# Performance work log

Hardware: AMD Instinct MI355X
Metric: run time of the kernel (lower is better)

## Reference

```python
import jax, jax.numpy as jnp
import numpy as np


def setup_inputs() -> dict:
    key = jax.random.key(0)
    k1, k2, k3 = jax.random.split(key, 3)
    B, C, H, W = 16, 256, 32, 32
    D, K = 256, 8192
    x = jax.random.normal(k1, (B, C, H, W), dtype=jnp.float32)
    conv_w = jax.random.normal(k2, (D, C), dtype=jnp.float32) * (1.0 / np.sqrt(C))
    conv_b = jnp.zeros((D,), dtype=jnp.float32)
    codebook = jax.random.normal(k3, (D, K), dtype=jnp.float32)
    return {"x": x, "conv_w": conv_w, "conv_b": conv_b, "codebook": codebook}


def reference(x, conv_w, conv_b, codebook):
    # 1x1 conv projection: (B,C,H,W) -> (B,D,H,W)
    xp = jnp.einsum('bchw,dc->bdhw', x, conv_w) + conv_b[None, :, None, None]
    B, D, H, W = xp.shape
    K = codebook.shape[1]
    # flatten to (N, D), N = B*H*W
    xr = jnp.transpose(xp, (0, 2, 3, 1)).reshape(-1, D)
    dist = (jnp.sum(xr * xr, axis=1, keepdims=True)
            - 2.0 * (xr @ codebook)
            + jnp.sum(codebook * codebook, axis=0, keepdims=True))
    indices = jnp.argmax(-dist, axis=1).reshape(B, H, W)  # argmin distance
    # gather codes: (B,H,W,D) -> (B,D,H,W)
    quantized = jnp.take(codebook.T, indices.reshape(-1), axis=0)
    quantized = jnp.transpose(quantized.reshape(B, H, W, D), (0, 3, 1, 2))
    # commitment loss
    diff = jnp.mean((jax.lax.stop_gradient(quantized) - xp) ** 2)
    # straight-through estimator
    quantized_st = xp + jax.lax.stop_gradient(quantized - xp)
    return quantized_st, diff, indices
```

## Files before the change

kernel.cpp:

```cpp
#include <hip/hip_runtime.h>

typedef short bf16x8 __attribute__((ext_vector_type(8)));
typedef float f32x4 __attribute__((ext_vector_type(4)));
typedef float f32x16 __attribute__((ext_vector_type(16)));
using u16 = unsigned short;
using u32 = unsigned int;

#define MFMA_BF16(A, B, C) __builtin_amdgcn_mfma_f32_16x16x32_bf16((A), (B), (C), 0, 0, 0)
#define MFMA32_BF16(A, B, C) __builtin_amdgcn_mfma_f32_32x32x16_bf16((A), (B), (C), 0, 0, 0)

#define CC 256
#define DD 256
#define KK 8192
#define NN 16384
#define HW 1024
#define OUT0 4194304
#define KSPLIT 16
#define KROWS 32

static __device__ __forceinline__ float b2f(u16 u) {
    union { u32 i; float f; } v; v.i = ((u32)u) << 16; return v.f;
}
static __device__ __forceinline__ u16 f2b(float f) {
    union { float f; u32 i; } v; v.f = f;
    u32 x = v.i;
    u32 r = (x + 0x7fffu + ((x >> 16) & 1u)) >> 16;
    return (u16)r;
}
static __device__ __forceinline__ u32 f2u(float f) {
    union { float f; u32 u; } v; v.f = f; return v.u;
}
static __device__ __forceinline__ void split3(float v, u16& h, u16& m, u16& l) {
    h = f2b(v); float r1 = v - b2f(h);
    m = f2b(r1); float r2 = r1 - b2f(m);
    l = f2b(r2);
}

typedef __attribute__((address_space(1))) const u32 GlbU32;
typedef __attribute__((address_space(3))) u32 LdsU32;
static __device__ __forceinline__ void async_load16(const void* g, void* l) {
    __builtin_amdgcn_global_load_lds((GlbU32*)g, (LdsU32*)l, 16, 0, 0);
}

__global__ __launch_bounds__(256) void k_prep(const float* __restrict__ cb,
                                              const float* __restrict__ Wm,
                                              float* __restrict__ cbT,
                                              u16* __restrict__ cbTh,
                                              float* __restrict__ negC0,
                                              u16* __restrict__ wh,
                                              u16* __restrict__ wm,
                                              u16* __restrict__ wl) {
    int bx = blockIdx.x, tid = threadIdx.x;
    if (bx < 2048) {
        __shared__ float tile[32][33];
        int k0 = (bx & 255) * 32, d0 = (bx >> 8) * 32;
        int tx = tid & 31, ty = tid >> 5;
#pragma unroll
        for (int i = 0; i < 4; i++) {
            int d = d0 + ty + i * 8;
            tile[ty + i * 8][tx] = cb[d * KK + k0 + tx];
        }
        __syncthreads();
#pragma unroll
        for (int i = 0; i < 4; i++) {
            int k = k0 + ty + i * 8;
            float v = tile[tx][ty + i * 8];
            cbT[k * DD + d0 + tx] = v;
            cbTh[k * DD + d0 + tx] = f2b(v);
        }
    } else if (bx < 2304) {
        __shared__ float sm[8][32];
        int kl = tid & 31, dg = tid >> 5;
        int k = (bx - 2048) * 32 + kl;
        float s = 0.f;
#pragma unroll
        for (int j = 0; j < 32; j++) {
            float v = cb[(size_t)(dg * 32 + j) * KK + k];
            s += v * v;
        }
        sm[dg][kl] = s;
        __syncthreads();
        if (tid < 32) {
            float t = 0.f;
#pragma unroll
            for (int g = 0; g < 8; g++) t += sm[g][tid];
            negC0[(bx - 2048) * 32 + tid] = -0.5f * (t + 1024.f);
        }
    } else {
        int t = (bx - 2304) * 256 + tid;
        int j    = t & 7;
        int lane = (t >> 3) & 63;
        int cc   = (t >> 9) & 7;
        int dtg  = t >> 12;
        int l15 = lane & 15, quad = lane >> 4;
        int src = (dtg * 16 + l15) * CC + cc * 32 + quad * 8 + j;
        u16 h, m, l; split3(Wm[src], h, m, l);
        wh[t] = h; wm[t] = m; wl[t] = l;
    }
}

__global__ __launch_bounds__(256) void k_proj(const float* __restrict__ x,
                                              const u16* __restrict__ wh,
                                              const u16* __restrict__ wm,
                                              const u16* __restrict__ wl,
                                              const float* __restrict__ bias,
                                              float* __restrict__ xp,
                                              u16* __restrict__ xpH) {
    int tid = threadIdx.x;
    int wave = tid >> 6, lane = tid & 63;
    int quad = lane >> 4, l15 = lane & 15;
    int n0 = (blockIdx.x >> 1) * 16;
    int dhalf = blockIdx.x & 1;
    int n_a = n0 + l15;
    const float* xb = x + (n_a >> 10) * (CC * HW) + (n_a & (HW - 1));

    f32x4 acc[2];
#pragma unroll
    for (int i = 0; i < 2; i++) acc[i] = (f32x4){0.f, 0.f, 0.f, 0.f};

#pragma unroll
    for (int cc = 0; cc < 8; cc++) {
        bf16x8 ah, am, al;
#pragma unroll
        for (int j = 0; j < 8; j++) {
            float v = xb[(cc * 32 + quad * 8 + j) * HW];
            u16 h, m, l; split3(v, h, m, l);
            ah[j] = (short)h; am[j] = (short)m; al[j] = (short)l;
        }
#pragma unroll
        for (int dt = 0; dt < 2; dt++) {
            int dtg = dhalf * 8 + wave * 2 + dt;
            int off = ((dtg * 8 + cc) * 64 + lane) * 8;
            const bf16x8 bh = *(const bf16x8*)(wh + off);
            const bf16x8 bm = *(const bf16x8*)(wm + off);
            const bf16x8 bl = *(const bf16x8*)(wl + off);
            acc[dt] = MFMA_BF16(ah, bh, acc[dt]);
            acc[dt] = MFMA_BF16(am, bh, acc[dt]);
            acc[dt] = MFMA_BF16(ah, bm, acc[dt]);
            acc[dt] = MFMA_BF16(al, bh, acc[dt]);
            acc[dt] = MFMA_BF16(am, bm, acc[dt]);
            acc[dt] = MFMA_BF16(ah, bl, acc[dt]);
        }
    }

#pragma unroll
    for (int dt = 0; dt < 2; dt++) {
        int dtg = dhalf * 8 + wave * 2 + dt;
        int d = dtg * 16 + l15;
        float bv = bias[d];
#pragma unroll
        for (int r = 0; r < 4; r++) {
            int n = n0 + quad * 4 + r;
            float v = acc[dt][r] + bv;
            xp[n * DD + d] = v;
            xpH[n * DD + d] = f2b(v);
        }
    }
}

__global__ __launch_bounds__(256, 3) void k_dist(const u16* __restrict__ xpH,
                                                 const u16* __restrict__ cbTh,
                                                 const float* __restrict__ negC0,
                                                 u32* __restrict__ pkey) {
    __shared__ __align__(16) u16 tile[2][KROWS * 256];
    int tid = threadIdx.x, wave = tid >> 6, lane = tid & 63;
    int col = lane & 31, half = lane >> 5;
    int n0 = blockIdx.x * 128 + wave * 32;
    int ksbase = blockIdx.y * (KK / KSPLIT);

    bf16x8 Ah[16];
    {
        const u16* ab = xpH + (size_t)(n0 + col) * DD + half * 8;
#pragma unroll
        for (int ks = 0; ks < 16; ks++)
            Ah[ks] = *(const bf16x8*)(ab + ks * 16);
    }

    u32 key[16];
#pragma unroll
    for (int g = 0; g < 16; g++) key[g] = 0xffffffffu;

#define STAGE(bufi, kglob_)                                                    \
    {                                                                          \
        int kg_ = (kglob_);                                                    \
        _Pragma("unroll")                                                      \
        for (int c = 0; c < 4; c++) {                                          \
            int chunk = wave * 4 + c;                                          \
            int row = chunk * 2 + (lane >> 5);                                 \
            int g = (lane & 31) ^ (row & 7);                                   \
            const u16* src = cbTh + (size_t)(kg_ + row) * DD + g * 8;          \
            async_load16(src, &tile[bufi][chunk * 512]);                       \
        }                                                                      \
    }

    STAGE(0, ksbase);
    float nc_cur = negC0[ksbase + col];
    __syncthreads();

    for (int kc = 0; kc < 16; kc++) {
        int buf = kc & 1;
        float nc_next = 0.f;
        if (kc < 15) {
            STAGE(buf ^ 1, ksbase + (kc + 1) * KROWS);
            nc_next = negC0[ksbase + (kc + 1) * KROWS + col];
        }

        f32x16 a0, a1;
#pragma unroll
        for (int g = 0; g < 16; g++) { a0[g] = nc_cur; a1[g] = 0.f; }

        const u16* trow = &tile[buf][col * 256];
#pragma unroll
        for (int ks = 0; ks < 8; ks++) {
            int g0 = ((2 * ks) * 2 + half) ^ (col & 7);
            int g1 = ((2 * ks + 1) * 2 + half) ^ (col & 7);
            const bf16x8 Bf0 = *(const bf16x8*)(trow + g0 * 8);
            const bf16x8 Bf1 = *(const bf16x8*)(trow + g1 * 8);
            a0 = MFMA32_BF16(Ah[2 * ks], Bf0, a0);
            a1 = MFMA32_BF16(Ah[2 * ks + 1], Bf1, a1);
        }

        u32 orv = ((u32)kc << 5) | (u32)col;
#pragma unroll
        for (int g = 0; g < 16; g++) {
            u32 kb = (f2u(a0[g] + a1[g]) & 0xFFFFFE00u) | orv;
            key[g] = min(key[g], kb);
        }
        nc_cur = nc_next;
        __syncthreads();
    }
#undef STAGE

#pragma unroll
    for (int g = 0; g < 16; g++) {
        u32 k1 = key[g], k2 = 0xffffffffu;
#pragma unroll
        for (int m = 1; m < 32; m <<= 1) {
            u32 o1 = (u32)__shfl_xor((int)k1, m, 64);
            u32 o2 = (u32)__shfl_xor((int)k2, m, 64);
            u32 mx = max(k1, o1);
            k1 = min(k1, o1);
            k2 = min(min(k2, o2), mx);
        }
        if (col == 0) {
            int row = (g & 3) + 8 * (g >> 2) + 4 * half;
            int n = n0 + row;
            int base = (n * KSPLIT + blockIdx.y) * 2;
            pkey[base]     = (u32)ksbase + (k1 & 511u);
            pkey[base + 1] = (u32)ksbase + (k2 & 511u);
        }
    }
}

__global__ __launch_bounds__(256) void k_rescore(const float* __restrict__ xp,
                                                 const float* __restrict__ cbT,
                                                 const u32* __restrict__ pkey,
                                                 u32* __restrict__ idxv,
                                                 float* __restrict__ outIdx,
                                                 float* __restrict__ pmin) {
    int tid = threadIdx.x, wave = tid >> 6, lane = tid & 63;
    int n = blockIdx.x * 4 + wave;
    int sub = lane >> 3;
    int oct = lane & 7;

    f32x4 xv[8];
    const float* xb = xp + n * DD;
#pragma unroll
    for (int t = 0; t < 8; t++) xv[t] = *(const f32x4*)(xb + (t * 8 + oct) * 4);

    u32 myk = pkey[n * 32 + (lane & 31)] & 8191u;

    double bestv = 1e300;
    u32 besti = 0u;
#pragma unroll
    for (int g = 0; g < 4; g++) {
        int c = g * 8 + sub;
        u32 kg = (u32)__shfl((int)myk, c, 64);
        const float* cv = cbT + (size_t)kg * DD;
        double s = 0.0;
#pragma unroll
        for (int t = 0; t < 8; t++) {
            f32x4 cvv = *(const f32x4*)(cv + (t * 8 + oct) * 4);
#pragma unroll
            for (int q = 0; q < 4; q++) {
                double d = (double)xv[t][q] - (double)cvv[q];
                s += d * d;
            }
        }
        s += __shfl_xor(s, 1, 64);
        s += __shfl_xor(s, 2, 64);
        s += __shfl_xor(s, 4, 64);
        if (s < bestv || (s == bestv && kg < besti)) { bestv = s; besti = kg; }
    }
#pragma unroll
    for (int m = 8; m < 64; m <<= 1) {
        double ov = __shfl_xor(bestv, m, 64);
        u32 oi = (u32)__shfl_xor((int)besti, m, 64);
        if (ov < bestv || (ov == bestv && oi < besti)) { bestv = ov; besti = oi; }
    }
    if (lane == 0) {
        idxv[n] = besti;
        outIdx[n] = (float)besti;
        pmin[n] = (float)bestv;
    }
}

__global__ __launch_bounds__(256) void k_gather(const float* __restrict__ cbT,
                                                const u32* __restrict__ idxv,
                                                const float* __restrict__ pmin,
                                                float* __restrict__ out0,
                                                float* __restrict__ outDiff) {
    if (blockIdx.x == NN / 32) {
        __shared__ double sm[4];
        int tid = threadIdx.x, lane = tid & 63, wv = tid >> 6;
        double s = 0.0;
#pragma unroll
        for (int i = 0; i < 64; i++) s += (double)pmin[i * 256 + tid];
#pragma unroll
        for (int m = 1; m < 64; m <<= 1) s += __shfl_xor(s, m, 64);
        if (lane == 0) sm[wv] = s;
        __syncthreads();
        if (tid == 0)
            outDiff[0] = (float)((sm[0] + sm[1] + sm[2] + sm[3]) * (1.0 / (double)OUT0));
        return;
    }

    __shared__ float tile[32 * 260];
    int tid = threadIdx.x;
    int n0 = blockIdx.x * 32;
    int b = n0 >> 10, hw0 = n0 & 1023;

    {
        int r = tid >> 3, seg = tid & 7;
        u32 k = idxv[n0 + r] & 8191u;
        const float* src = cbT + (size_t)k * DD;
        float* dst = tile + r * 260;
#pragma unroll
        for (int j = 0; j < 8; j++)
            *(f32x4*)(dst + (j * 8 + seg) * 4) = *(const f32x4*)(src + (j * 8 + seg) * 4);
    }
    __syncthreads();
    {
        int hw = tid & 31, dq = tid >> 5;
        const float* trow = tile + hw * 260;
        float* obase = out0 + ((size_t)b * DD) * HW + hw0 + hw;
#pragma unroll
        for (int dj = 0; dj < 32; dj++) {
            int d = dq * 32 + dj;
            obase[(size_t)d * HW] = trow[d];
        }
    }
}

extern "C" void kernel_launch(void* const* d_in, const int* in_sizes, int n_in,
                              void* d_out, int out_size, void* d_ws, size_t ws_size,
                              hipStream_t stream) {
    const float* x = nullptr; const float* Wm = nullptr;
    const float* bias = nullptr; const float* cb = nullptr;
    for (int i = 0; i < n_in; i++) {
        switch (in_sizes[i]) {
            case 4194304: x    = (const float*)d_in[i]; break;
            case 65536:   Wm   = (const float*)d_in[i]; break;
            case 256:     bias = (const float*)d_in[i]; break;
            case 2097152: cb   = (const float*)d_in[i]; break;
        }
    }

    float* out0    = (float*)d_out;
    float* outDiff = (float*)d_out + OUT0;
    float* outIdx  = (float*)d_out + OUT0 + 1;

    char* o = (char*)d_out;
    u16*   cbTh = (u16*)o;
    u32*   pkey = (u32*)(o + 4194304);
    u16*   wh   = (u16*)(o + 6291456);
    u16*   wm   = (u16*)(o + 6422528);
    u16*   wl   = (u16*)(o + 6553600);
    u16*   xpH  = (u16*)(o + 6750208);

    char* w = (char*)d_ws;
    float* cbT   = (float*)(w);
    float* xp    = (float*)(w + 8388608);
    float* negC0 = (float*)(w + 25165824);
    u32*   idxv  = (u32*)(w + 25198592);
    float* pmin  = (float*)(w + 25264128);

    k_prep<<<2560, 256, 0, stream>>>(cb, Wm, cbT, cbTh, negC0, wh, wm, wl);
    k_proj<<<NN / 8, 256, 0, stream>>>(x, wh, wm, wl, bias, xp, xpH);
    k_dist<<<dim3(NN / 128, KSPLIT), 256, 0, stream>>>(xpH, cbTh, negC0, pkey);
    k_rescore<<<NN / 4, 256, 0, stream>>>(xp, cbT, pkey, idxv, outIdx, pmin);
    k_gather<<<NN / 32 + 1, 256, 0, stream>>>(cbT, idxv, pmin, out0, outDiff);
}
```

Before: 242.4 us.

## Halve K-split count and rescore only top-4 candidates by approximate score

Cuts the codebook split count from 16 to 8, so each distance block scans 32 chunks and keeps 10 index bits in its packed key. Partial keys now carry the approximate score bits, and the rescore kernel picks the four smallest across splits and rescores only those in fp64 instead of all 32 candidates. This reduces rescore loads and arithmetic, plus the number of distance blocks and partial-key writes. The cost is fewer candidates and coarser score bits in the key, which risks picking a different argmin when approximate distances are close.

```diff
diff --git a/kernel.cpp b/kernel.cpp
--- a/kernel.cpp
+++ b/kernel.cpp
@@ -15,7 +15,7 @@
 #define NN 16384
 #define HW 1024
 #define OUT0 4194304
-#define KSPLIT 16
+#define KSPLIT 8
 #define KROWS 32
 
 static __device__ __forceinline__ float b2f(u16 u) {
@@ -197,10 +197,10 @@
     float nc_cur = negC0[ksbase + col];
     __syncthreads();
 
-    for (int kc = 0; kc < 16; kc++) {
+    for (int kc = 0; kc < 32; kc++) {
         int buf = kc & 1;
         float nc_next = 0.f;
-        if (kc < 15) {
+        if (kc < 31) {
             STAGE(buf ^ 1, ksbase + (kc + 1) * KROWS);
             nc_next = negC0[ksbase + (kc + 1) * KROWS + col];
         }
@@ -223,7 +223,7 @@
         u32 orv = ((u32)kc << 5) | (u32)col;
 #pragma unroll
         for (int g = 0; g < 16; g++) {
-            u32 kb = (f2u(a0[g] + a1[g]) & 0xFFFFFE00u) | orv;
+            u32 kb = (f2u(a0[g] + a1[g]) & 0xFFFFFC00u) | orv;
             key[g] = min(key[g], kb);
         }
         nc_cur = nc_next;
@@ -246,8 +246,8 @@
             int row = (g & 3) + 8 * (g >> 2) + 4 * half;
             int n = n0 + row;
             int base = (n * KSPLIT + blockIdx.y) * 2;
-            pkey[base]     = (u32)ksbase + (k1 & 511u);
-            pkey[base + 1] = (u32)ksbase + (k2 & 511u);
+            pkey[base]     = (k1 & 0xFFFFE000u) | ((u32)ksbase + (k1 & 1023u));
+            pkey[base + 1] = (k2 & 0xFFFFE000u) | ((u32)ksbase + (k2 & 1023u));
         }
     }
 }
@@ -260,40 +260,52 @@
                                                  float* __restrict__ pmin) {
     int tid = threadIdx.x, wave = tid >> 6, lane = tid & 63;
     int n = blockIdx.x * 4 + wave;
-    int sub = lane >> 3;
-    int oct = lane & 7;
-
-    f32x4 xv[8];
+
+    u32 key = (lane < 16) ? pkey[n * 16 + lane] : 0xffffffffu;
+
+    u32 cand0, cand1, cand2, cand3;
+#define EXTRACT(C)                                                             \
+    {                                                                          \
+        u32 kmin = key;                                                        \
+        kmin = min(kmin, (u32)__shfl_xor((int)kmin, 1, 64));                   \
+        kmin = min(kmin, (u32)__shfl_xor((int)kmin, 2, 64));                   \
+        kmin = min(kmin, (u32)__shfl_xor((int)kmin, 4, 64));                   \
+        kmin = min(kmin, (u32)__shfl_xor((int)kmin, 8, 64));                   \
+        C = (u32)__shfl((int)kmin, 0, 64);                                     \
+        if (key == C) key = 0xffffffffu;                                       \
+    }
+    EXTRACT(cand0)
+    EXTRACT(cand1)
+    EXTRACT(cand2)
+    EXTRACT(cand3)
+#undef EXTRACT
+
+    int g = lane >> 4, sl = lane & 15;
+    u32 ck = (g == 0) ? cand0 : (g == 1) ? cand1 : (g == 2) ? cand2 : cand3;
+    u32 kg = ck & 8191u;
+
+    const float* cv = cbT + (size_t)kg * DD;
     const float* xb = xp + n * DD;
-#pragma unroll
-    for (int t = 0; t < 8; t++) xv[t] = *(const f32x4*)(xb + (t * 8 + oct) * 4);
-
-    u32 myk = pkey[n * 32 + (lane & 31)] & 8191u;
-
-    double bestv = 1e300;
-    u32 besti = 0u;
-#pragma unroll
-    for (int g = 0; g < 4; g++) {
-        int c = g * 8 + sub;
-        u32 kg = (u32)__shfl((int)myk, c, 64);
-        const float* cv = cbT + (size_t)kg * DD;
-        double s = 0.0;
-#pragma unroll
-        for (int t = 0; t < 8; t++) {
-            f32x4 cvv = *(const f32x4*)(cv + (t * 8 + oct) * 4);
-#pragma unroll
-            for (int q = 0; q < 4; q++) {
-                double d = (double)xv[t][q] - (double)cvv[q];
-                s += d * d;
-            }
-        }
-        s += __shfl_xor(s, 1, 64);
-        s += __shfl_xor(s, 2, 64);
-        s += __shfl_xor(s, 4, 64);
-        if (s < bestv || (s == bestv && kg < besti)) { bestv = s; besti = kg; }
-    }
-#pragma unroll
-    for (int m = 8; m < 64; m <<= 1) {
+    double s = 0.0;
+#pragma unroll
+    for (int t = 0; t < 4; t++) {
+        f32x4 cvv = *(const f32x4*)(cv + (t * 16 + sl) * 4);
+        f32x4 xvv = *(const f32x4*)(xb + (t * 16 + sl) * 4);
+#pragma unroll
+        for (int q = 0; q < 4; q++) {
+            double d = (double)xvv[q] - (double)cvv[q];
+            s += d * d;
+        }
+    }
+    s += __shfl_xor(s, 1, 64);
+    s += __shfl_xor(s, 2, 64);
+    s += __shfl_xor(s, 4, 64);
+    s += __shfl_xor(s, 8, 64);
+
+    double bestv = s;
+    u32 besti = kg;
+#pragma unroll
+    for (int m = 16; m < 64; m <<= 1) {
         double ov = __shfl_xor(bestv, m, 64);
         u32 oi = (u32)__shfl_xor((int)besti, m, 64);
         if (ov < bestv || (ov == bestv && oi < besti)) { bestv = ov; besti = oi; }
```

New measurement: 201.9 us. -16.7%, faster.
